# Optimization experiments

Hardware: AMD Instinct MI355X
Metric: run time of the kernel (lower is better)

The kernel has to match this reference:

```python
import jax, jax.numpy as jnp
import numpy as np

T, K, H, B = 4096, 64, 128, 128


def setup_inputs() -> dict:
    key = jax.random.key(0)
    ks = jax.random.split(key, 6)
    stdv = 1.0 / np.sqrt(H)  # matches init_weights_random: uniform(-stdv, stdv)
    x = jax.random.normal(ks[0], (T, K, B), dtype=jnp.float32)
    init_hidden_states = jax.random.normal(ks[1], (H, B), dtype=jnp.float32)
    A1 = jax.random.uniform(ks[2], (K, K), minval=-stdv, maxval=stdv, dtype=jnp.float32)
    A2 = jax.random.uniform(ks[3], (K, H), minval=-stdv, maxval=stdv, dtype=jnp.float32)
    A3 = jax.random.uniform(ks[4], (H, K), minval=-stdv, maxval=stdv, dtype=jnp.float32)
    A4 = jax.random.uniform(ks[5], (H, H), minval=-stdv, maxval=stdv, dtype=jnp.float32)
    return {"x": x, "init_hidden_states": init_hidden_states,
            "A1": A1, "A2": A2, "A3": A3, "A4": A4}


def reference(x, init_hidden_states, A1, A2, A3, A4):
    # x: [T, K, B]; hidden: [H, B]
    # known_t = A1 @ x_t + A2 @ h_{t-1};  h_t = A3 @ x_t + A4 @ h_{t-1}
    def step(h, x_t):
        known = A1 @ x_t + A2 @ h
        h_new = A3 @ x_t + A4 @ h
        return h_new, (known, h_new)

    _, (known_seq, hidden_seq) = jax.lax.scan(step, init_hidden_states, x)
    return known_seq, hidden_seq  # [T, K, B], [T, H, B]
```

## Files before the change

### kernel.cpp

```cpp
#include <hip/hip_runtime.h>
#include <stdint.h>

typedef _Float16 half8 __attribute__((ext_vector_type(8)));
typedef float floatx4 __attribute__((ext_vector_type(4)));

constexpr int T  = 4096;
constexpr int KD = 64;
constexpr int HD = 128;
constexpr int BD = 128;
constexpr int KT = KD + HD;
constexpr int CH = 128;
constexpr int LS = T / CH;
constexpr int BC = 32;
constexpr int NSP = BD / BC;
constexpr int G  = 8;
constexpr int NG = CH / G;

static_assert(CH * LS == T, "");
static_assert(NG * G == CH, "");

constexpr size_t W_OFF  = 0;
constexpr size_t M_OFF  = 73728;
constexpr size_t M8_OFF = M_OFF + 32768;
constexpr size_t U_OFF  = M8_OFF + 32768;
constexpr size_t S_OFF  = U_OFF + (size_t)CH * BD * HD * 2;
constexpr size_t AGG_OFF = S_OFF + (size_t)CH * BD * HD * 2;

__device__ __forceinline__ unsigned short f2h(float v) {
  _Float16 h = (_Float16)v;
  return __builtin_bit_cast(unsigned short, h);
}
__device__ __forceinline__ float h2f(unsigned short u) {
  return (float)__builtin_bit_cast(_Float16, u);
}
__device__ __forceinline__ unsigned pack2(float a, float b) {
  return (unsigned)f2h(a) | ((unsigned)f2h(b) << 16);
}
__device__ __forceinline__ int swz(int g, int n) {
  return (g & ~7) | ((g & 7) ^ (n & 7));
}

__global__ __launch_bounds__(256) void prep_kernel(
    const float* __restrict__ A1, const float* __restrict__ A2,
    const float* __restrict__ A3, const float* __restrict__ A4,
    unsigned short* __restrict__ Wf, unsigned short* __restrict__ Mf,
    unsigned short* __restrict__ M8f) {
  if (blockIdx.x < 36) {
    for (int e = 0; e < 4; ++e) {
      int id = blockIdx.x * 1024 + e * 256 + threadIdx.x;
      int r = id / KT, cc = id % KT;
      float v;
      if (r < KD) v = (cc < KD) ? A1[r * KD + cc] : A2[r * HD + (cc - KD)];
      else        v = (cc < KD) ? A3[(r - KD) * KD + cc] : A4[(r - KD) * HD + (cc - KD)];
      Wf[id] = f2h(v);
    }
    return;
  }
  __shared__ __align__(16) unsigned short Mrow[HD * HD];
  __shared__ __align__(16) unsigned short Mcol[HD * HD];
  const int tid = threadIdx.x;
  for (int j = 0; j < 64; ++j) {
    int id = j * 256 + tid;
    int r = id >> 7, cc = id & 127;
    unsigned short hb = f2h(A4[id]);
    Mrow[id] = hb;
    Mcol[cc * HD + r] = hb;
  }
  __syncthreads();
  const int wv = tid >> 6, ln = tid & 63, l15 = ln & 15, q = ln >> 4;
  for (int it = 0; it < 8; ++it) {
    half8 af[2][4];
#pragma unroll
    for (int m = 0; m < 2; ++m)
#pragma unroll
      for (int kt = 0; kt < 4; ++kt)
        af[m][kt] = *reinterpret_cast<const half8*>(
            &Mrow[(wv * 32 + m * 16 + l15) * HD + kt * 32 + q * 8]);
    floatx4 acc[2][8];
#pragma unroll
    for (int m = 0; m < 2; ++m)
#pragma unroll
      for (int nt = 0; nt < 8; ++nt) {
        floatx4 z = {0.f, 0.f, 0.f, 0.f};
        acc[m][nt] = z;
      }
#pragma unroll
    for (int kt = 0; kt < 4; ++kt)
#pragma unroll
      for (int nt = 0; nt < 8; ++nt) {
        half8 bf = *reinterpret_cast<const half8*>(
            &Mcol[(nt * 16 + l15) * HD + kt * 32 + q * 8]);
#pragma unroll
        for (int m = 0; m < 2; ++m)
          acc[m][nt] = __builtin_amdgcn_mfma_f32_16x16x32_f16(af[m][kt], bf, acc[m][nt], 0, 0, 0);
      }
    __syncthreads();
#pragma unroll
    for (int m = 0; m < 2; ++m)
#pragma unroll
      for (int nt = 0; nt < 8; ++nt) {
        int Rb = wv * 32 + m * 16 + q * 4;
        int col = nt * 16 + l15;
#pragma unroll
        for (int r = 0; r < 4; ++r) {
          unsigned short hb = f2h(acc[m][nt][r]);
          Mrow[(Rb + r) * HD + col] = hb;
          Mcol[col * HD + (Rb + r)] = hb;
        }
      }
    __syncthreads();
    if (it == 4) {
      for (int j = 0; j < 64; ++j) {
        int id = j * 256 + tid;
        Mf[id] = Mrow[id];
      }
    }
    if (it == 7) {
      for (int j = 0; j < 64; ++j) {
        int id = j * 256 + tid;
        M8f[id] = Mrow[id];
      }
    }
  }
}

template <bool WRITE_OUT, bool ZERO_INIT>
__global__ __launch_bounds__(256, 2) void rnn_pass(
    const float* __restrict__ x, const unsigned short* __restrict__ Wf,
    const float* __restrict__ init_h, const unsigned short* __restrict__ s16,
    unsigned short* __restrict__ u16, float* __restrict__ out_known,
    float* __restrict__ out_hidden) {
  const int c = blockIdx.x / NSP;
  const int col0 = (blockIdx.x % NSP) * BC;
  const int tid = threadIdx.x;
  const int wv = tid >> 6;
  const int ln = tid & 63;
  const int l15 = ln & 15;
  const int q = ln >> 4;

  __shared__ __align__(16) unsigned short Bsh[BC * KT];

  half8 afrag[3][6];
#pragma unroll
  for (int m = 0; m < 3; ++m)
#pragma unroll
    for (int kt = 0; kt < 6; ++kt)
      afrag[m][kt] = *reinterpret_cast<const half8*>(
          Wf + (wv * 48 + m * 16 + l15) * KT + kt * 32 + q * 8);

  {
    int b = tid & 31;
    int r0 = (tid >> 5) * 16;
    if (ZERO_INIT) {
      uint4 z = {0u, 0u, 0u, 0u};
      *reinterpret_cast<uint4*>(&Bsh[b * KT + swz((KD + r0) >> 3, b) * 8]) = z;
      *reinterpret_cast<uint4*>(&Bsh[b * KT + swz((KD + r0 + 8) >> 3, b) * 8]) = z;
    } else if (c == 0) {
      float hv[16];
#pragma unroll
      for (int j = 0; j < 16; ++j)
        hv[j] = init_h[(size_t)(r0 + j) * BD + col0 + b];
#pragma unroll
      for (int hf = 0; hf < 2; ++hf) {
        int o = hf * 8;
        uint4 v;
        v.x = pack2(hv[o + 0], hv[o + 1]);
        v.y = pack2(hv[o + 2], hv[o + 3]);
        v.z = pack2(hv[o + 4], hv[o + 5]);
        v.w = pack2(hv[o + 6], hv[o + 7]);
        *reinterpret_cast<uint4*>(&Bsh[b * KT + swz((KD + r0 + o) >> 3, b) * 8]) = v;
      }
    } else {
      const unsigned short* sp = s16 + ((size_t)c * BD + col0 + b) * HD + r0;
      uint4 v0 = *reinterpret_cast<const uint4*>(sp);
      uint4 v1 = *reinterpret_cast<const uint4*>(sp + 8);
      *reinterpret_cast<uint4*>(&Bsh[b * KT + swz((KD + r0) >> 3, b) * 8]) = v0;
      *reinterpret_cast<uint4*>(&Bsh[b * KT + swz((KD + r0 + 8) >> 3, b) * 8]) = v1;
    }
  }
  {
    int b = tid & 31;
    int k0 = (tid >> 5) * 8;
    const float* xp = x + (size_t)(c * LS) * KD * BD + col0 + b;
    float xv[8];
#pragma unroll
    for (int j = 0; j < 8; ++j) xv[j] = xp[(size_t)(k0 + j) * BD];
    uint4 v;
    v.x = pack2(xv[0], xv[1]);
    v.y = pack2(xv[2], xv[3]);
    v.z = pack2(xv[4], xv[5]);
    v.w = pack2(xv[6], xv[7]);
    *reinterpret_cast<uint4*>(&Bsh[b * KT + swz(k0 >> 3, b) * 8]) = v;
  }
  __syncthreads();

  for (int i = 0; i < LS; ++i) {
    const int t = c * LS + i;
    float xv[8];
    const int b = tid & 31;
    const int xk0 = (tid >> 5) * 8;
    if (i + 1 < LS) {
      const float* xp = x + (size_t)(t + 1) * KD * BD + col0 + b;
#pragma unroll
      for (int j = 0; j < 8; ++j) xv[j] = xp[(size_t)(xk0 + j) * BD];
    }
    floatx4 acc[3][2];
#pragma unroll
    for (int m = 0; m < 3; ++m)
#pragma unroll
      for (int nt = 0; nt < 2; ++nt) {
        floatx4 z = {0.f, 0.f, 0.f, 0.f};
        acc[m][nt] = z;
      }
#pragma unroll
    for (int kt = 0; kt < 6; ++kt)
#pragma unroll
      for (int nt = 0; nt < 2; ++nt) {
        int n = nt * 16 + l15;
        half8 bf = *reinterpret_cast<const half8*>(
            &Bsh[n * KT + swz(kt * 4 + q, n) * 8]);
#pragma unroll
        for (int m = 0; m < 3; ++m)
          acc[m][nt] = __builtin_amdgcn_mfma_f32_16x16x32_f16(
              afrag[m][kt], bf, acc[m][nt], 0, 0, 0);
      }
    __syncthreads();
#pragma unroll
    for (int m = 0; m < 3; ++m) {
      int Rb = wv * 48 + m * 16 + q * 4;
#pragma unroll
      for (int nt = 0; nt < 2; ++nt) {
        int col = col0 + nt * 16 + l15;
        if (Rb < KD) {
          if (WRITE_OUT) {
            float* kp = out_known + (size_t)t * KD * BD + (size_t)Rb * BD + col;
#pragma unroll
            for (int r = 0; r < 4; ++r) kp[(size_t)r * BD] = acc[m][nt][r];
          }
        } else {
          int hr = Rb - KD;
          if (WRITE_OUT) {
            float* hp = out_hidden + (size_t)t * HD * BD + (size_t)hr * BD + col;
#pragma unroll
            for (int r = 0; r < 4; ++r) hp[(size_t)r * BD] = acc[m][nt][r];
          }
          if (!WRITE_OUT && i == LS - 1) {
            unsigned short* up = u16 + ((size_t)c * BD + col) * HD + hr;
            uint2 pku;
            pku.x = pack2(acc[m][nt][0], acc[m][nt][1]);
            pku.y = pack2(acc[m][nt][2], acc[m][nt][3]);
            *reinterpret_cast<uint2*>(up) = pku;
          }
          int n = nt * 16 + l15;
          uint2 pk;
          pk.x = pack2(acc[m][nt][0], acc[m][nt][1]);
          pk.y = pack2(acc[m][nt][2], acc[m][nt][3]);
          *reinterpret_cast<uint2*>(&Bsh[n * KT + swz(Rb >> 3, n) * 8 + (Rb & 7)]) = pk;
        }
      }
    }
    if (i + 1 < LS) {
      uint4 v;
      v.x = pack2(xv[0], xv[1]);
      v.y = pack2(xv[2], xv[3]);
      v.z = pack2(xv[4], xv[5]);
      v.w = pack2(xv[6], xv[7]);
      *reinterpret_cast<uint4*>(&Bsh[b * KT + swz(xk0 >> 3, b) * 8]) = v;
    }
    __syncthreads();
  }
}

__device__ __forceinline__ void load_mfrag(const unsigned short* Mp, half8 (&af)[2][4],
                                           int wv, int l15, int q) {
#pragma unroll
  for (int m = 0; m < 2; ++m)
#pragma unroll
    for (int kt = 0; kt < 4; ++kt)
      af[m][kt] = *reinterpret_cast<const half8*>(
          Mp + (wv * 32 + m * 16 + l15) * HD + kt * 32 + q * 8);
}

__device__ __forceinline__ void stage_h_f32(const float* __restrict__ hsrc,
                                            unsigned short* Hsh, int col0, int tid) {
  int b = tid & 31;
  int r0 = (tid >> 5) * 16;
  float hv[16];
#pragma unroll
  for (int j = 0; j < 16; ++j)
    hv[j] = hsrc[(size_t)(r0 + j) * BD + col0 + b];
#pragma unroll
  for (int hf = 0; hf < 2; ++hf) {
    int o = hf * 8;
    uint4 v;
    v.x = pack2(hv[o + 0], hv[o + 1]);
    v.y = pack2(hv[o + 2], hv[o + 3]);
    v.z = pack2(hv[o + 4], hv[o + 5]);
    v.w = pack2(hv[o + 6], hv[o + 7]);
    *reinterpret_cast<uint4*>(&Hsh[b * HD + swz((r0 + o) >> 3, b) * 8]) = v;
  }
}

__device__ __forceinline__ void stage_h_f16(const unsigned short* __restrict__ sp16,
                                            unsigned short* Hsh, int col0, int tid) {
  int b = tid & 31;
  int r0 = (tid >> 5) * 16;
  const unsigned short* sp = sp16 + ((size_t)col0 + b) * HD + r0;
  uint4 v0 = *reinterpret_cast<const uint4*>(sp);
  uint4 v1 = *reinterpret_cast<const uint4*>(sp + 8);
  *reinterpret_cast<uint4*>(&Hsh[b * HD + swz(r0 >> 3, b) * 8]) = v0;
  *reinterpret_cast<uint4*>(&Hsh[b * HD + swz((r0 + 8) >> 3, b) * 8]) = v1;
}

template <bool WRITE_S>
__device__ __forceinline__ void comb_step(
    const half8 (&af)[2][4], unsigned short* Hsh,
    const unsigned short* __restrict__ uc, unsigned short* __restrict__ sc,
    int col0, int wv, int l15, int q) {
  floatx4 acc[2][2];
#pragma unroll
  for (int m = 0; m < 2; ++m)
#pragma unroll
    for (int nt = 0; nt < 2; ++nt) {
      floatx4 z = {0.f, 0.f, 0.f, 0.f};
      acc[m][nt] = z;
    }
#pragma unroll
  for (int kt = 0; kt < 4; ++kt)
#pragma unroll
    for (int nt = 0; nt < 2; ++nt) {
      int n = nt * 16 + l15;
      half8 bf = *reinterpret_cast<const half8*>(
          &Hsh[n * HD + swz(kt * 4 + q, n) * 8]);
#pragma unroll
      for (int m = 0; m < 2; ++m)
        acc[m][nt] = __builtin_amdgcn_mfma_f32_16x16x32_f16(af[m][kt], bf, acc[m][nt], 0, 0, 0);
    }
  __syncthreads();
#pragma unroll
  for (int m = 0; m < 2; ++m) {
    int Rb = wv * 32 + m * 16 + q * 4;
#pragma unroll
    for (int nt = 0; nt < 2; ++nt) {
      int col = col0 + nt * 16 + l15;
      uint2 uv = *reinterpret_cast<const uint2*>(uc + (size_t)col * HD + Rb);
      float s0 = acc[m][nt][0] + h2f((unsigned short)(uv.x & 0xffff));
      float s1 = acc[m][nt][1] + h2f((unsigned short)(uv.x >> 16));
      float s2 = acc[m][nt][2] + h2f((unsigned short)(uv.y & 0xffff));
      float s3 = acc[m][nt][3] + h2f((unsigned short)(uv.y >> 16));
      uint2 pk;
      pk.x = pack2(s0, s1);
      pk.y = pack2(s2, s3);
      if (WRITE_S) *reinterpret_cast<uint2*>(sc + (size_t)col * HD + Rb) = pk;
      int n = nt * 16 + l15;
      *reinterpret_cast<uint2*>(&Hsh[n * HD + swz(Rb >> 3, n) * 8 + (Rb & 7)]) = pk;
    }
  }
  __syncthreads();
}

__global__ __launch_bounds__(256) void combine_agg(
    const unsigned short* __restrict__ Mf, const unsigned short* __restrict__ u16,
    unsigned short* __restrict__ agg16) {
  const int j = blockIdx.x / NSP;
  const int col0 = (blockIdx.x % NSP) * BC;
  const int tid = threadIdx.x;
  const int wv = tid >> 6, ln = tid & 63, l15 = ln & 15, q = ln >> 4;
  __shared__ __align__(16) unsigned short Hsh[BC * HD];
  half8 af[2][4];
  load_mfrag(Mf, af, wv, l15, q);
  for (int jj = tid; jj < BC * HD; jj += 256) Hsh[jj] = 0;
  __syncthreads();
  for (int i = 0; i < G; ++i) {
    const unsigned short* uc = u16 + (size_t)(j * G + i) * BD * HD;
    if (i == G - 1)
      comb_step<true>(af, Hsh, uc, agg16 + (size_t)j * BD * HD, col0, wv, l15, q);
    else
      comb_step<false>(af, Hsh, uc, nullptr, col0, wv, l15, q);
  }
}

__global__ __launch_bounds__(256) void combine_serial(
    const unsigned short* __restrict__ M8f, const float* __restrict__ init_h,
    const unsigned short* __restrict__ agg16, unsigned short* __restrict__ s16) {
  const int col0 = blockIdx.x * BC;
  const int tid = threadIdx.x;
  const int wv = tid >> 6, ln = tid & 63, l15 = ln & 15, q = ln >> 4;
  __shared__ __align__(16) unsigned short Hsh[BC * HD];
  half8 af[2][4];
  load_mfrag(M8f, af, wv, l15, q);
  stage_h_f32(init_h, Hsh, col0, tid);
  __syncthreads();
  for (int j = 0; j < NG - 1; ++j)
    comb_step<true>(af, Hsh, agg16 + (size_t)j * BD * HD,
                    s16 + (size_t)(j + 1) * G * BD * HD, col0, wv, l15, q);
}

__global__ __launch_bounds__(256) void combine_fill(
    const unsigned short* __restrict__ Mf, const float* __restrict__ init_h,
    const unsigned short* __restrict__ u16, unsigned short* __restrict__ s16) {
  const int j = blockIdx.x / NSP;
  const int col0 = (blockIdx.x % NSP) * BC;
  const int tid = threadIdx.x;
  const int wv = tid >> 6, ln = tid & 63, l15 = ln & 15, q = ln >> 4;
  __shared__ __align__(16) unsigned short Hsh[BC * HD];
  half8 af[2][4];
  load_mfrag(Mf, af, wv, l15, q);
  if (j == 0) stage_h_f32(init_h, Hsh, col0, tid);
  else        stage_h_f16(s16 + (size_t)j * G * BD * HD, Hsh, col0, tid);
  __syncthreads();
  for (int i = 0; i < G - 1; ++i)
    comb_step<true>(af, Hsh, u16 + (size_t)(j * G + i) * BD * HD,
                    s16 + (size_t)(j * G + i + 1) * BD * HD, col0, wv, l15, q);
}

extern "C" void kernel_launch(void* const* d_in, const int* in_sizes, int n_in,
                              void* d_out, int out_size, void* d_ws, size_t ws_size,
                              hipStream_t stream) {
  const float* x  = (const float*)d_in[0];
  const float* ih = (const float*)d_in[1];
  const float* A1 = (const float*)d_in[2];
  const float* A2 = (const float*)d_in[3];
  const float* A3 = (const float*)d_in[4];
  const float* A4 = (const float*)d_in[5];
  char* ws = (char*)d_ws;
  unsigned short* Wf  = (unsigned short*)(ws + W_OFF);
  unsigned short* Mf  = (unsigned short*)(ws + M_OFF);
  unsigned short* M8f = (unsigned short*)(ws + M8_OFF);
  unsigned short* u16 = (unsigned short*)(ws + U_OFF);
  unsigned short* s16 = (unsigned short*)(ws + S_OFF);
  unsigned short* agg16 = (unsigned short*)(ws + AGG_OFF);
  float* known = (float*)d_out;
  float* hidden = known + (size_t)T * KD * BD;

  prep_kernel<<<37, 256, 0, stream>>>(A1, A2, A3, A4, Wf, Mf, M8f);
  rnn_pass<false, true><<<(CH - 1) * NSP, 256, 0, stream>>>(
      x, Wf, nullptr, nullptr, u16, nullptr, nullptr);
  combine_agg<<<(NG - 1) * NSP, 256, 0, stream>>>(Mf, u16, agg16);
  combine_serial<<<NSP, 256, 0, stream>>>(M8f, ih, agg16, s16);
  combine_fill<<<NG * NSP, 256, 0, stream>>>(Mf, ih, u16, s16);
  rnn_pass<true, false><<<CH * NSP, 256, 0, stream>>>(
      x, Wf, ih, s16, nullptr, known, hidden);
}
```

Baseline: 645.4 us.

## Fuse the five scan-stage launches into one cooperative persistent kernel

The chunk pass, the aggregate, serial and fill combine stages, and the final output pass are merged into one cooperative kernel. Blocks loop over tasks and a grid-wide sync separates each phase. This removes four kernel launches and the gaps between them. In exchange it adds grid-sync overhead, assumes 256 CUs to size the grid from occupancy, and leaves most blocks idle during the 4-block serial phase.

```diff
diff --git a/kernel.cpp b/kernel.cpp
--- a/kernel.cpp
+++ b/kernel.cpp
@@ -1,5 +1,8 @@
 #include <hip/hip_runtime.h>
+#include <hip/hip_cooperative_groups.h>
 #include <stdint.h>
+
+namespace cg = cooperative_groups;
 
 typedef _Float16 half8 __attribute__((ext_vector_type(8)));
 typedef float floatx4 __attribute__((ext_vector_type(4)));
@@ -125,29 +128,12 @@
 }
 
 template <bool WRITE_OUT, bool ZERO_INIT>
-__global__ __launch_bounds__(256, 2) void rnn_pass(
-    const float* __restrict__ x, const unsigned short* __restrict__ Wf,
+__device__ __forceinline__ void rnn_chunk(
+    int c, int col0, const float* __restrict__ x, const half8 (&afrag)[3][6],
     const float* __restrict__ init_h, const unsigned short* __restrict__ s16,
     unsigned short* __restrict__ u16, float* __restrict__ out_known,
-    float* __restrict__ out_hidden) {
-  const int c = blockIdx.x / NSP;
-  const int col0 = (blockIdx.x % NSP) * BC;
-  const int tid = threadIdx.x;
-  const int wv = tid >> 6;
-  const int ln = tid & 63;
-  const int l15 = ln & 15;
-  const int q = ln >> 4;
-
-  __shared__ __align__(16) unsigned short Bsh[BC * KT];
-
-  half8 afrag[3][6];
-#pragma unroll
-  for (int m = 0; m < 3; ++m)
-#pragma unroll
-    for (int kt = 0; kt < 6; ++kt)
-      afrag[m][kt] = *reinterpret_cast<const half8*>(
-          Wf + (wv * 48 + m * 16 + l15) * KT + kt * 32 + q * 8);
-
+    float* __restrict__ out_hidden, unsigned short* Bsh,
+    int tid, int wv, int l15, int q) {
   {
     int b = tid & 31;
     int r0 = (tid >> 5) * 16;
@@ -359,59 +345,95 @@
   __syncthreads();
 }
 
-__global__ __launch_bounds__(256) void combine_agg(
-    const unsigned short* __restrict__ Mf, const unsigned short* __restrict__ u16,
-    unsigned short* __restrict__ agg16) {
-  const int j = blockIdx.x / NSP;
-  const int col0 = (blockIdx.x % NSP) * BC;
+__global__ __launch_bounds__(256, 2) void fused_kernel(
+    const float* __restrict__ x, const unsigned short* __restrict__ Wf,
+    const unsigned short* __restrict__ Mf, const unsigned short* __restrict__ M8f,
+    const float* __restrict__ init_h, unsigned short* __restrict__ u16,
+    unsigned short* __restrict__ s16, unsigned short* __restrict__ agg16,
+    float* __restrict__ out_known, float* __restrict__ out_hidden) {
+  cg::grid_group grid = cg::this_grid();
   const int tid = threadIdx.x;
   const int wv = tid >> 6, ln = tid & 63, l15 = ln & 15, q = ln >> 4;
-  __shared__ __align__(16) unsigned short Hsh[BC * HD];
-  half8 af[2][4];
-  load_mfrag(Mf, af, wv, l15, q);
-  for (int jj = tid; jj < BC * HD; jj += 256) Hsh[jj] = 0;
-  __syncthreads();
-  for (int i = 0; i < G; ++i) {
-    const unsigned short* uc = u16 + (size_t)(j * G + i) * BD * HD;
-    if (i == G - 1)
-      comb_step<true>(af, Hsh, uc, agg16 + (size_t)j * BD * HD, col0, wv, l15, q);
-    else
-      comb_step<false>(af, Hsh, uc, nullptr, col0, wv, l15, q);
-  }
-}
-
-__global__ __launch_bounds__(256) void combine_serial(
-    const unsigned short* __restrict__ M8f, const float* __restrict__ init_h,
-    const unsigned short* __restrict__ agg16, unsigned short* __restrict__ s16) {
-  const int col0 = blockIdx.x * BC;
-  const int tid = threadIdx.x;
-  const int wv = tid >> 6, ln = tid & 63, l15 = ln & 15, q = ln >> 4;
-  __shared__ __align__(16) unsigned short Hsh[BC * HD];
-  half8 af[2][4];
-  load_mfrag(M8f, af, wv, l15, q);
-  stage_h_f32(init_h, Hsh, col0, tid);
-  __syncthreads();
-  for (int j = 0; j < NG - 1; ++j)
-    comb_step<true>(af, Hsh, agg16 + (size_t)j * BD * HD,
-                    s16 + (size_t)(j + 1) * G * BD * HD, col0, wv, l15, q);
-}
-
-__global__ __launch_bounds__(256) void combine_fill(
-    const unsigned short* __restrict__ Mf, const float* __restrict__ init_h,
-    const unsigned short* __restrict__ u16, unsigned short* __restrict__ s16) {
-  const int j = blockIdx.x / NSP;
-  const int col0 = (blockIdx.x % NSP) * BC;
-  const int tid = threadIdx.x;
-  const int wv = tid >> 6, ln = tid & 63, l15 = ln & 15, q = ln >> 4;
-  __shared__ __align__(16) unsigned short Hsh[BC * HD];
-  half8 af[2][4];
-  load_mfrag(Mf, af, wv, l15, q);
-  if (j == 0) stage_h_f32(init_h, Hsh, col0, tid);
-  else        stage_h_f16(s16 + (size_t)j * G * BD * HD, Hsh, col0, tid);
-  __syncthreads();
-  for (int i = 0; i < G - 1; ++i)
-    comb_step<true>(af, Hsh, u16 + (size_t)(j * G + i) * BD * HD,
-                    s16 + (size_t)(j * G + i + 1) * BD * HD, col0, wv, l15, q);
+  const int nb = gridDim.x;
+  __shared__ __align__(16) unsigned short smem[BC * KT];
+
+  {
+    half8 afrag[3][6];
+#pragma unroll
+    for (int m = 0; m < 3; ++m)
+#pragma unroll
+      for (int kt = 0; kt < 6; ++kt)
+        afrag[m][kt] = *reinterpret_cast<const half8*>(
+            Wf + (wv * 48 + m * 16 + l15) * KT + kt * 32 + q * 8);
+    for (int task = blockIdx.x; task < (CH - 1) * NSP; task += nb)
+      rnn_chunk<false, true>(task / NSP, (task % NSP) * BC, x, afrag, nullptr,
+                             nullptr, u16, nullptr, nullptr, smem, tid, wv, l15, q);
+  }
+  __threadfence();
+  grid.sync();
+
+  {
+    half8 af[2][4];
+    load_mfrag(Mf, af, wv, l15, q);
+    for (int task = blockIdx.x; task < (NG - 1) * NSP; task += nb) {
+      const int j = task / NSP, col0 = (task % NSP) * BC;
+      for (int jj = tid; jj < BC * HD; jj += 256) smem[jj] = 0;
+      __syncthreads();
+      for (int i = 0; i < G; ++i) {
+        const unsigned short* uc = u16 + (size_t)(j * G + i) * BD * HD;
+        if (i == G - 1)
+          comb_step<true>(af, smem, uc, agg16 + (size_t)j * BD * HD, col0, wv, l15, q);
+        else
+          comb_step<false>(af, smem, uc, nullptr, col0, wv, l15, q);
+      }
+    }
+  }
+  __threadfence();
+  grid.sync();
+
+  {
+    half8 af[2][4];
+    load_mfrag(M8f, af, wv, l15, q);
+    for (int task = blockIdx.x; task < NSP; task += nb) {
+      const int col0 = task * BC;
+      stage_h_f32(init_h, smem, col0, tid);
+      __syncthreads();
+      for (int j = 0; j < NG - 1; ++j)
+        comb_step<true>(af, smem, agg16 + (size_t)j * BD * HD,
+                        s16 + (size_t)(j + 1) * G * BD * HD, col0, wv, l15, q);
+    }
+  }
+  __threadfence();
+  grid.sync();
+
+  {
+    half8 af[2][4];
+    load_mfrag(Mf, af, wv, l15, q);
+    for (int task = blockIdx.x; task < NG * NSP; task += nb) {
+      const int j = task / NSP, col0 = (task % NSP) * BC;
+      if (j == 0) stage_h_f32(init_h, smem, col0, tid);
+      else        stage_h_f16(s16 + (size_t)j * G * BD * HD, smem, col0, tid);
+      __syncthreads();
+      for (int i = 0; i < G - 1; ++i)
+        comb_step<true>(af, smem, u16 + (size_t)(j * G + i) * BD * HD,
+                        s16 + (size_t)(j * G + i + 1) * BD * HD, col0, wv, l15, q);
+    }
+  }
+  __threadfence();
+  grid.sync();
+
+  {
+    half8 afrag[3][6];
+#pragma unroll
+    for (int m = 0; m < 3; ++m)
+#pragma unroll
+      for (int kt = 0; kt < 6; ++kt)
+        afrag[m][kt] = *reinterpret_cast<const half8*>(
+            Wf + (wv * 48 + m * 16 + l15) * KT + kt * 32 + q * 8);
+    for (int task = blockIdx.x; task < CH * NSP; task += nb)
+      rnn_chunk<true, false>(task / NSP, (task % NSP) * BC, x, afrag, init_h,
+                             s16, nullptr, out_known, out_hidden, smem, tid, wv, l15, q);
+  }
 }
 
 extern "C" void kernel_launch(void* const* d_in, const int* in_sizes, int n_in,
@@ -434,11 +456,20 @@
   float* hidden = known + (size_t)T * KD * BD;
 
   prep_kernel<<<37, 256, 0, stream>>>(A1, A2, A3, A4, Wf, Mf, M8f);
-  rnn_pass<false, true><<<(CH - 1) * NSP, 256, 0, stream>>>(
-      x, Wf, nullptr, nullptr, u16, nullptr, nullptr);
-  combine_agg<<<(NG - 1) * NSP, 256, 0, stream>>>(Mf, u16, agg16);
-  combine_serial<<<NSP, 256, 0, stream>>>(M8f, ih, agg16, s16);
-  combine_fill<<<NG * NSP, 256, 0, stream>>>(Mf, ih, u16, s16);
-  rnn_pass<true, false><<<CH * NSP, 256, 0, stream>>>(
-      x, Wf, ih, s16, nullptr, known, hidden);
-}
+
+  static int nblk = -1;
+  if (nblk < 0) {
+    int occ = 0;
+    (void)hipOccupancyMaxActiveBlocksPerMultiprocessor(&occ, (const void*)fused_kernel,
+                                                       256, 0);
+    if (occ < 1) occ = 1;
+    long cap = (long)occ * 256;
+    nblk = (int)(cap < (long)CH * NSP ? cap : (long)CH * NSP);
+  }
+
+  void* kargs[] = {
+      (void*)&x, (void*)&Wf, (void*)&Mf, (void*)&M8f, (void*)&ih,
+      (void*)&u16, (void*)&s16, (void*)&agg16, (void*)&known, (void*)&hidden};
+  (void)hipLaunchCooperativeKernel((const void*)fused_kernel, dim3(nblk), dim3(256),
+                                   kargs, 0, stream);
+}
```

Result: slower. 871.7 us (+35.1%).
